# Performance work log

Measured on AMD Instinct MI355X. Metric: run time of the kernel, lower is better.

Reference implementation:

```python
import jax, jax.numpy as jnp
import numpy as np

B, C_IN, C_OUT, C_KEY, N = 8, 512, 512, 256, 2048


def setup_inputs() -> dict:
    key = jax.random.key(0)
    k1, k2, k3, k4 = jax.random.split(key, 4)
    x = jax.random.normal(k1, (B, C_IN, N), dtype=jnp.float32)
    # Conv1d(kernel=1, bias=False) weights -> plain linear maps over channel dim
    Wq = jax.random.normal(k2, (C_KEY, C_IN), dtype=jnp.float32) * (1.0 / np.sqrt(C_IN))
    Wk = jax.random.normal(k3, (C_KEY, C_IN), dtype=jnp.float32) * (1.0 / np.sqrt(C_IN))
    Wv = jax.random.normal(k4, (C_OUT, C_IN), dtype=jnp.float32) * (1.0 / np.sqrt(C_IN))
    return {"x": x, "Wq": Wq, "Wk": Wk, "Wv": Wv}


def reference(x, Wq, Wk, Wv):
    # 1x1 conv projections: [B, C, N] -> [B, Ck/Co, N]
    q = jnp.einsum("oc,bcn->bon", Wq, x)
    k = jnp.einsum("oc,bcn->bon", Wk, x)
    v = jnpqv = jnp.einsum("oc,bcn->bon", Wv, x)
    # sim_map[b,i,j] = sum_c k[b,c,i] * q[b,c,j]  (unscaled)
    sim = jnp.einsum("bci,bcj->bij", k, q)  # [B, N, N]
    attn = jax.nn.softmax(sim, axis=-1)
    # out = value @ sim_map, then permute(0,2,1) -> [B, N, C_out]
    out = jnp.einsum("bck,bkm->bmc", jnpqv, attn)
    return out
```

## Files before the change

### kernel.cpp

```cpp
#include <hip/hip_runtime.h>

typedef _Float16 half8 __attribute__((ext_vector_type(8)));
typedef _Float16 half4v __attribute__((ext_vector_type(4)));
typedef _Float16 half2v __attribute__((ext_vector_type(2)));
typedef float f32x4 __attribute__((ext_vector_type(4)));

#define ASYNC_CP16(gp, lp)                                       \
  __builtin_amdgcn_global_load_lds(                              \
      (const __attribute__((address_space(1))) void*)(gp),       \
      (__attribute__((address_space(3))) void*)(lp), 16, 0, 0)

__global__ __launch_bounds__(256) void conv_w(const float* __restrict__ Wq,
                                              const float* __restrict__ Wk,
                                              const float* __restrict__ Wv,
                                              _Float16* __restrict__ Wb) {
  int idx = blockIdx.x * 256 + threadIdx.x;
  int row = idx >> 9;
  float v;
  if (row < 256)      v = Wq[idx];
  else if (row < 512) v = Wk[idx - 256 * 512];
  else                v = Wv[idx - 512 * 512];
  Wb[idx] = (_Float16)v;
}

__global__ __launch_bounds__(256) void conv_xT(const float* __restrict__ x,
                                               _Float16* __restrict__ xT) {
  __shared__ float T[32][33];
  const int b = blockIdx.z;
  const int n0 = blockIdx.x * 32, c0 = blockIdx.y * 32;
  const int t = threadIdx.x;
  const float* xb = x + (size_t)b * 512 * 2048;
  const int n2 = t & 15, cr = t >> 4;
#pragma unroll
  for (int r = 0; r < 2; r++) {
    int c = cr + r * 16;
    float2 v = *(const float2*)&xb[(size_t)(c0 + c) * 2048 + n0 + n2 * 2];
    T[c][n2 * 2] = v.x;
    T[c][n2 * 2 + 1] = v.y;
  }
  __syncthreads();
  _Float16* xtb = xT + (size_t)b * 2048 * 512;
  const int c2 = t & 15, nr = t >> 4;
#pragma unroll
  for (int r = 0; r < 2; r++) {
    int n = nr + r * 16;
    half2v h;
    h[0] = (_Float16)T[c2 * 2][n];
    h[1] = (_Float16)T[c2 * 2 + 1][n];
    *(half2v*)&xtb[(size_t)(n0 + n) * 512 + c0 + c2 * 2] = h;
  }
}

template <typename OutT, int BUFS, int MODE>
__global__ __launch_bounds__(256) void gemm_nt(
    const _Float16* __restrict__ A, const _Float16* __restrict__ B,
    OutT* __restrict__ C, OutT* __restrict__ C2, int K, int lda, int ldb,
    int ldc, int ldc2, long sA, long sB, long sC, float* __restrict__ pm,
    float* __restrict__ ps) {
  A += (size_t)blockIdx.z * sA;
  B += (size_t)blockIdx.z * sB;
  C += (size_t)blockIdx.z * sC;
  if constexpr (MODE == 1) C2 += (size_t)blockIdx.z * sC;
  const int m_blk = blockIdx.y * 128, n_blk = blockIdx.x * 128;

  __shared__ _Float16 As[BUFS][4096];
  __shared__ _Float16 Bs[BUFS][4096];

  const int t = threadIdx.x;
  const int lane = t & 63, wave = t >> 6;
  const int quad = lane >> 4, l16 = lane & 15;
  const int wm = (wave & 1) * 64, wn = (wave >> 1) * 64;

  const int srow = 16 * wave + (lane >> 2);
  const int schunk = (lane & 3) ^ ((lane >> 3) & 3);
  const _Float16* gA0 = A + (size_t)(m_blk + srow) * lda + schunk * 8;
  const _Float16* gA1 = gA0 + (size_t)64 * lda;
  const _Float16* gB0 = B + (size_t)(n_blk + srow) * ldb + schunk * 8;
  const _Float16* gB1 = gB0 + (size_t)64 * ldb;
  const int lofs = wave * 512 + lane * 8;

  const int rchunk = (quad ^ ((l16 >> 1) & 3)) * 8;

  f32x4 acc[4][4] = {};

#pragma unroll
  for (int pb = 0; pb < BUFS - 1; pb++) {
    if (pb * 32 < K) {
      ASYNC_CP16(gA0 + pb * 32, &As[pb][lofs]);
      ASYNC_CP16(gA1 + pb * 32, &As[pb][lofs + 2048]);
      ASYNC_CP16(gB0 + pb * 32, &Bs[pb][lofs]);
      ASYNC_CP16(gB1 + pb * 32, &Bs[pb][lofs + 2048]);
    }
  }

  int ib = 0;
  for (int k0 = 0; k0 < K; k0 += 32) {
    if constexpr (BUFS == 3) {
      if (k0 + 32 < K)
        asm volatile("s_waitcnt vmcnt(4)\n\ts_barrier" ::: "memory");
      else
        asm volatile("s_waitcnt vmcnt(0)\n\ts_barrier" ::: "memory");
    } else {
      asm volatile("s_waitcnt vmcnt(0)\n\ts_barrier" ::: "memory");
    }
    if (k0 + (BUFS - 1) * 32 < K) {
      int nb = ib + BUFS - 1;
      if (nb >= BUFS) nb -= BUFS;
      const int ko = k0 + (BUFS - 1) * 32;
      ASYNC_CP16(gA0 + ko, &As[nb][lofs]);
      ASYNC_CP16(gA1 + ko, &As[nb][lofs + 2048]);
      ASYNC_CP16(gB0 + ko, &Bs[nb][lofs]);
      ASYNC_CP16(gB1 + ko, &Bs[nb][lofs + 2048]);
    }
    half8 af[4], bf[4];
#pragma unroll
    for (int i = 0; i < 4; i++) {
      af[i] = *(const half8*)&As[ib][(wm + i * 16 + l16) * 32 + rchunk];
      bf[i] = *(const half8*)&Bs[ib][(wn + i * 16 + l16) * 32 + rchunk];
    }
#pragma unroll
    for (int i = 0; i < 4; i++)
#pragma unroll
      for (int j = 0; j < 4; j++)
        acc[i][j] =
            __builtin_amdgcn_mfma_f32_16x16x32_f16(af[i], bf[j], acc[i][j], 0, 0, 0);
    ib++;
    if (ib == BUFS) ib = 0;
  }

#pragma unroll
  for (int i = 0; i < 4; i++) {
    const int m0 = m_blk + wm + i * 16 + quad * 4;
#pragma unroll
    for (int j = 0; j < 4; j++) {
      const int n0 = n_blk + wn + j * 16 + l16;
      if constexpr (MODE == 1) {
        if (m_blk < 512) {
          half4v h;
#pragma unroll
          for (int r = 0; r < 4; r++) h[r] = (_Float16)acc[i][j][r];
          *(half4v*)&C[(size_t)n0 * ldc + m0] = h;
        } else {
#pragma unroll
          for (int r = 0; r < 4; r++)
            C2[(size_t)(m0 - 512 + r) * ldc2 + n0] = (OutT)acc[i][j][r];
        }
      } else if constexpr (MODE == 2) {
#pragma unroll
        for (int r = 0; r < 4; r++) {
          _Float16 h = (_Float16)acc[i][j][r];
          C[(size_t)(m0 + r) * ldc + n0] = h;
          acc[i][j][r] = (float)h;
        }
      } else {
#pragma unroll
        for (int r = 0; r < 4; r++)
          C[(size_t)(m0 + r) * ldc + n0] = (OutT)acc[i][j][r];
      }
    }
  }

  if constexpr (MODE == 2) {
    __shared__ float sred[128][2][2];
    float pM[4], pS[4];
#pragma unroll
    for (int j = 0; j < 4; j++) {
      float mx = acc[0][j][0];
#pragma unroll
      for (int i = 0; i < 4; i++)
#pragma unroll
        for (int r = 0; r < 4; r++) mx = fmaxf(mx, acc[i][j][r]);
      mx = fmaxf(mx, __shfl_xor(mx, 16, 64));
      mx = fmaxf(mx, __shfl_xor(mx, 32, 64));
      float es = 0.f;
#pragma unroll
      for (int i = 0; i < 4; i++)
#pragma unroll
        for (int r = 0; r < 4; r++) es += __expf(acc[i][j][r] - mx);
      es += __shfl_xor(es, 16, 64);
      es += __shfl_xor(es, 32, 64);
      pM[j] = mx;
      pS[j] = es;
    }
    if (quad == 0) {
#pragma unroll
      for (int j = 0; j < 4; j++) {
        sred[wn + j * 16 + l16][wave & 1][0] = pM[j];
        sred[wn + j * 16 + l16][wave & 1][1] = pS[j];
      }
    }
    __syncthreads();
    if (t < 128) {
      float m0 = sred[t][0][0], s0 = sred[t][0][1];
      float m1 = sred[t][1][0], s1 = sred[t][1][1];
      float M = fmaxf(m0, m1);
      float S = s0 * __expf(m0 - M) + s1 * __expf(m1 - M);
      size_t o = ((size_t)blockIdx.z * 16 + blockIdx.y) * 2048 + n_blk + t;
      pm[o] = M;
      ps[o] = S;
    }
  }
}

__global__ __launch_bounds__(256) void colstats2(const float* __restrict__ pm,
                                                 const float* __restrict__ ps,
                                                 float* __restrict__ shift) {
  const int idx = blockIdx.x * 256 + threadIdx.x;
  const int b = idx >> 11, col = idx & 2047;
  const float* pmb = pm + (size_t)b * 16 * 2048 + col;
  const float* psb = ps + (size_t)b * 16 * 2048 + col;
  float m = -3.0e38f;
#pragma unroll
  for (int i = 0; i < 16; i++) m = fmaxf(m, pmb[(size_t)i * 2048]);
  float s = 0.f;
#pragma unroll
  for (int i = 0; i < 16; i++)
    s += psb[(size_t)i * 2048] * __expf(pmb[(size_t)i * 2048] - m);
  shift[idx] = m + __logf(s);
}

__global__ __launch_bounds__(256) void attnscale(_Float16* __restrict__ simH,
                                                 const float* __restrict__ shift) {
  const size_t b = blockIdx.y;
  const size_t g = (size_t)blockIdx.x * 256 + threadIdx.x;
  const int col = (int)(g & 255) * 8;
  _Float16* p = simH + b * (2048ull * 2048) + g * 8;
  half8 h = *(const half8*)p;
  f32x4 s0 = *(const f32x4*)(shift + b * 2048 + col);
  f32x4 s1 = *(const f32x4*)(shift + b * 2048 + col + 4);
  half8 o;
#pragma unroll
  for (int i = 0; i < 4; i++) {
    o[i] = (_Float16)__expf((float)h[i] - s0[i]);
    o[i + 4] = (_Float16)__expf((float)h[i + 4] - s1[i]);
  }
  *(half8*)p = o;
}

extern "C" void kernel_launch(void* const* d_in, const int* in_sizes, int n_in,
                              void* d_out, int out_size, void* d_ws,
                              size_t ws_size, hipStream_t stream) {
  const float* x = (const float*)d_in[0];
  const float* Wq = (const float*)d_in[1];
  const float* Wk = (const float*)d_in[2];
  const float* Wv = (const float*)d_in[3];
  float* out = (float*)d_out;

  char* p = (char*)d_ws;
  auto alloc = [&](size_t bytes) -> char* {
    char* r = p;
    p += (bytes + 255) & ~(size_t)255;
    return r;
  };
  const size_t NB = 8, N = 2048, CIN = 512, CO = 512;
  _Float16* Wb = (_Float16*)alloc(1024 * 512 * sizeof(_Float16));
  _Float16* xT = (_Float16*)alloc(NB * N * CIN * sizeof(_Float16));
  _Float16* qkT = (_Float16*)alloc(NB * N * 512 * sizeof(_Float16));
  _Float16* v = (_Float16*)alloc(NB * CO * N * sizeof(_Float16));
  size_t base_used = (size_t)(p - (char*)d_ws);

  const size_t per_b =
      (size_t)N * N * 2 + 2 * 16 * N * 4 + N * 4 + 8192;
  int cb = 8;
  while (cb > 1 && base_used + (size_t)cb * per_b > ws_size) cb >>= 1;
  _Float16* simH = (_Float16*)alloc((size_t)cb * N * N * 2);
  float* pm = (float*)alloc((size_t)cb * 16 * N * 4);
  float* ps = (float*)alloc((size_t)cb * 16 * N * 4);
  float* shift = (float*)alloc((size_t)cb * N * 4);

  conv_w<<<dim3(1024 * 512 / 256), 256, 0, stream>>>(Wq, Wk, Wv, Wb);
  conv_xT<<<dim3(64, 16, 8), 256, 0, stream>>>(x, xT);

  gemm_nt<_Float16, 3, 1><<<dim3(16, 8, 8), 256, 0, stream>>>(
      Wb, xT, qkT, v, 512, 512, 512, 512, 2048, 0, (long)(N * CIN),
      (long)(N * 512), nullptr, nullptr);

  for (int b0 = 0; b0 < 8; b0 += cb) {
    const _Float16* qT = qkT + (size_t)b0 * N * 512;
    const _Float16* kT = qkT + (size_t)b0 * N * 512 + 256;
    gemm_nt<_Float16, 2, 2><<<dim3(16, 16, cb), 256, 0, stream>>>(
        qT, kT, simH, nullptr, 256, 512, 512, 2048, 0, (long)(N * 512),
        (long)(N * 512), (long)(N * N), pm, ps);
    colstats2<<<dim3(cb * 8), 256, 0, stream>>>(pm, ps, shift);
    attnscale<<<dim3(2048, cb), 256, 0, stream>>>(simH, shift);
    gemm_nt<float, 3, 0><<<dim3(4, 16, cb), 256, 0, stream>>>(
        simH, v + (size_t)b0 * CO * N, out + (size_t)b0 * N * CO, nullptr,
        2048, 2048, 2048, 512, 0, (long)(N * N), (long)(CO * N),
        (long)(N * CO), nullptr, nullptr);
  }
}
```

Before: 229.3 us.

## Fuse softmax exponent scaling into attention-value GEMM A-tile load

Removes the separate attnscale pass, which read and rewrote the full fp16 similarity matrix. The exponentiation with the per-column shift now happens while A tiles are staged into shared memory, inside a new dedicated GEMM with 128x128 tiles, double-buffered LDS and async loads for V. The block index is remapped so that, when all eight batches run at once, neighbouring blocks belong to different batches. This saves a full-matrix memory round trip and a launch, at the cost of putting the exp arithmetic and synchronous global loads for A inside the GEMM's main loop.

```diff
diff --git a/kernel.cpp b/kernel.cpp
--- a/kernel.cpp
+++ b/kernel.cpp
@@ -219,22 +219,110 @@
   shift[idx] = m + __logf(s);
 }
 
-__global__ __launch_bounds__(256) void attnscale(_Float16* __restrict__ simH,
-                                                 const float* __restrict__ shift) {
-  const size_t b = blockIdx.y;
-  const size_t g = (size_t)blockIdx.x * 256 + threadIdx.x;
-  const int col = (int)(g & 255) * 8;
-  _Float16* p = simH + b * (2048ull * 2048) + g * 8;
-  half8 h = *(const half8*)p;
-  f32x4 s0 = *(const f32x4*)(shift + b * 2048 + col);
-  f32x4 s1 = *(const f32x4*)(shift + b * 2048 + col + 4);
-  half8 o;
+__global__ __launch_bounds__(256) void gemm_av(const _Float16* __restrict__ A,
+                                               const _Float16* __restrict__ V,
+                                               const float* __restrict__ shift,
+                                               float* __restrict__ C,
+                                               int cbatch) {
+  int lin = blockIdx.x, z, idx;
+  if (cbatch == 8) {
+    z = lin & 7;
+    idx = lin >> 3;
+  } else {
+    z = lin >> 6;
+    idx = lin & 63;
+  }
+  const int n_blk = (idx & 3) * 128;
+  const int m_blk = (idx >> 2) * 128;
+  A += (size_t)z * 2048 * 2048;
+  V += (size_t)z * 512 * 2048;
+  shift += (size_t)z * 2048;
+  C += (size_t)z * 2048 * 512;
+
+  __shared__ _Float16 As[2][4096];
+  __shared__ _Float16 Bs[2][4096];
+
+  const int t = threadIdx.x;
+  const int lane = t & 63, wave = t >> 6;
+  const int quad = lane >> 4, l16 = lane & 15;
+  const int wm = (wave & 1) * 64, wn = (wave >> 1) * 64;
+
+  const int srow = 16 * wave + (lane >> 2);
+  const int schunk = (lane & 3) ^ ((lane >> 3) & 3);
+  const _Float16* gA0 = A + (size_t)(m_blk + srow) * 2048 + schunk * 8;
+  const _Float16* gA1 = gA0 + (size_t)64 * 2048;
+  const _Float16* gB0 = V + (size_t)(n_blk + srow) * 2048 + schunk * 8;
+  const _Float16* gB1 = gB0 + (size_t)64 * 2048;
+  const float* gS = shift + schunk * 8;
+  const int lofs = wave * 512 + lane * 8;
+  const int rchunk = (quad ^ ((l16 >> 1) & 3)) * 8;
+
+  f32x4 acc[4][4] = {};
+
+  auto expw = [](half8 a, f32x4 s0, f32x4 s1) -> half8 {
+    half8 o;
+#pragma unroll
+    for (int j = 0; j < 4; j++) {
+      o[j] = (_Float16)__expf((float)a[j] - s0[j]);
+      o[j + 4] = (_Float16)__expf((float)a[j + 4] - s1[j]);
+    }
+    return o;
+  };
+
+  ASYNC_CP16(gB0, &Bs[0][lofs]);
+  ASYNC_CP16(gB1, &Bs[0][lofs + 2048]);
+  {
+    half8 a0 = *(const half8*)gA0;
+    half8 a1 = *(const half8*)gA1;
+    f32x4 s0 = *(const f32x4*)gS;
+    f32x4 s1 = *(const f32x4*)(gS + 4);
+    *(half8*)&As[0][lofs] = expw(a0, s0, s1);
+    *(half8*)&As[0][lofs + 2048] = expw(a1, s0, s1);
+  }
+  __syncthreads();
+
+  int ib = 0;
+  for (int k0 = 0; k0 < 2048; k0 += 32, ib ^= 1) {
+    half8 a0, a1;
+    f32x4 s0, s1;
+    const bool more = (k0 + 32 < 2048);
+    if (more) {
+      ASYNC_CP16(gB0 + k0 + 32, &Bs[ib ^ 1][lofs]);
+      ASYNC_CP16(gB1 + k0 + 32, &Bs[ib ^ 1][lofs + 2048]);
+      a0 = *(const half8*)(gA0 + k0 + 32);
+      a1 = *(const half8*)(gA1 + k0 + 32);
+      s0 = *(const f32x4*)(gS + k0 + 32);
+      s1 = *(const f32x4*)(gS + k0 + 36);
+    }
+    half8 af[4], bf[4];
+#pragma unroll
+    for (int i = 0; i < 4; i++) {
+      af[i] = *(const half8*)&As[ib][(wm + i * 16 + l16) * 32 + rchunk];
+      bf[i] = *(const half8*)&Bs[ib][(wn + i * 16 + l16) * 32 + rchunk];
+    }
+#pragma unroll
+    for (int i = 0; i < 4; i++)
+#pragma unroll
+      for (int j = 0; j < 4; j++)
+        acc[i][j] =
+            __builtin_amdgcn_mfma_f32_16x16x32_f16(af[i], bf[j], acc[i][j], 0, 0, 0);
+    if (more) {
+      *(half8*)&As[ib ^ 1][lofs] = expw(a0, s0, s1);
+      *(half8*)&As[ib ^ 1][lofs + 2048] = expw(a1, s0, s1);
+    }
+    __syncthreads();
+  }
+
 #pragma unroll
   for (int i = 0; i < 4; i++) {
-    o[i] = (_Float16)__expf((float)h[i] - s0[i]);
-    o[i + 4] = (_Float16)__expf((float)h[i + 4] - s1[i]);
-  }
-  *(half8*)p = o;
+    const int m0 = m_blk + wm + i * 16 + quad * 4;
+#pragma unroll
+    for (int j = 0; j < 4; j++) {
+      const int n0 = n_blk + wn + j * 16 + l16;
+#pragma unroll
+      for (int r = 0; r < 4; r++) C[(size_t)(m0 + r) * 512 + n0] = acc[i][j][r];
+    }
+  }
 }
 
 extern "C" void kernel_launch(void* const* d_in, const int* in_sizes, int n_in,
@@ -259,8 +347,7 @@
   _Float16* v = (_Float16*)alloc(NB * CO * N * sizeof(_Float16));
   size_t base_used = (size_t)(p - (char*)d_ws);
 
-  const size_t per_b =
-      (size_t)N * N * 2 + 2 * 16 * N * 4 + N * 4 + 8192;
+  const size_t per_b = (size_t)N * N * 2 + 2 * 16 * N * 4 + N * 4 + 8192;
   int cb = 8;
   while (cb > 1 && base_used + (size_t)cb * per_b > ws_size) cb >>= 1;
   _Float16* simH = (_Float16*)alloc((size_t)cb * N * N * 2);
@@ -282,10 +369,7 @@
         qT, kT, simH, nullptr, 256, 512, 512, 2048, 0, (long)(N * 512),
         (long)(N * 512), (long)(N * N), pm, ps);
     colstats2<<<dim3(cb * 8), 256, 0, stream>>>(pm, ps, shift);
-    attnscale<<<dim3(2048, cb), 256, 0, stream>>>(simH, shift);
-    gemm_nt<float, 3, 0><<<dim3(4, 16, cb), 256, 0, stream>>>(
-        simH, v + (size_t)b0 * CO * N, out + (size_t)b0 * N * CO, nullptr,
-        2048, 2048, 2048, 512, 0, (long)(N * N), (long)(CO * N),
-        (long)(N * CO), nullptr, nullptr);
-  }
-}
+    gemm_av<<<dim3(64 * cb), 256, 0, stream>>>(
+        simH, v + (size_t)b0 * CO * N, shift, out + (size_t)b0 * N * CO, cb);
+  }
+}
```

Measured after the change: 225.5 us. About the same (-1.7%).
